# Performance work log

Measured on AMD Instinct MI355X. Metric: run time of the kernel, lower is better.

Reference implementation:

```python
import jax, jax.numpy as jnp
import numpy as np
from jax import lax

IN_CH, FEAT, EMB, P = 384, 256, 32, 64
OUT_CH = (256, 512, 1024, 1024)
EPS_BN = 1e-5


def _conv(x, w, b, stride=1, pad=1, groups=1):
    # x: (B,C,H,W), w: (O, C//groups, kh, kw) torch OIHW layout
    y = lax.conv_general_dilated(x, w, (stride, stride), ((pad, pad), (pad, pad)),
                                 dimension_numbers=('NCHW', 'OIHW', 'NCHW'),
                                 feature_group_count=groups)
    return y + b[None, :, None, None]


def _bn(x, g, b, m, v):
    scale = (g / jnp.sqrt(v + EPS_BN))[None, :, None, None]
    return (x - m[None, :, None, None]) * scale + b[None, :, None, None]


def _convT_block(x, w, b, k):
    # ConvTranspose2d with kernel_size == stride == k, padding 0 (non-overlapping)
    # w: (C_in, C_out, k, k) torch layout
    B, C, H, W = x.shape
    O = w.shape[1]
    y = jnp.einsum('bchw,coij->bohiwj', x, w).reshape(B, O, H * k, W * k)
    return y + b[None, :, None, None]


def _resize_ac(x, oh, ow):
    # bilinear interpolation, align_corners=True; x: (B,C,H,W)
    H, W = x.shape[-2], x.shape[-1]
    def idx(n_in, n_out):
        c = jnp.arange(n_out, dtype=x.dtype) * ((n_in - 1) / max(n_out - 1, 1))
        i0 = jnp.clip(jnp.floor(c).astype(jnp.int32), 0, max(n_in - 2, 0))
        return i0, c - i0.astype(x.dtype)
    if oh != H:
        i0, t = idx(H, oh)
        x = x[:, :, i0, :] * (1.0 - t)[:, None] + x[:, :, jnp.minimum(i0 + 1, H - 1), :] * t[:, None]
    if ow != W:
        j0, t = idx(W, ow)
        x = x[:, :, :, j0] * (1.0 - t) + x[:, :, :, jnp.minimum(j0 + 1, W - 1)] * t
    return x


def _avg3(x):
    # F.avg_pool2d(k=3, s=1, p=1) with count_include_pad=True -> always /9
    s = lax.reduce_window(x, jnp.float32(0.0), lax.add, (1, 1, 3, 3), (1, 1, 1, 1),
                          ((0, 0), (0, 0), (1, 1), (1, 1)))
    return s / 9.0


def _forward(tokens0, tokens1, tokens2, tokens3,
             proj_w0, proj_b0, proj_w1, proj_b1, proj_w2, proj_b2, proj_w3, proj_b3,
             up_w0, up_b0, up_w1, up_b1, down_w3, down_b3,
             fuse_w, fuse_b,
             pe_w1, pe_b1, pe_bn_g, pe_bn_b, pe_bn_m, pe_bn_v, pe_w2, pe_b2,
             prototypes, prototype_biases, bias_scale,
             smooth_w, smooth_b,
             head_w1, head_b1, hbn1_g, hbn1_b, hbn1_m, hbn1_v,
             head_w2, head_b2, hbn2_g, hbn2_b, hbn2_m, hbn2_v,
             head_w3, head_b3, residual_scale,
             patch_h, patch_w):
    B = tokens0.shape[0]
    toks = (tokens0, tokens1, tokens2, tokens3)
    proj = ((proj_w0, proj_b0), (proj_w1, proj_b1), (proj_w2, proj_b2), (proj_w3, proj_b3))
    feats = []
    for t, (w, b) in zip(toks, proj):
        x = t.transpose(0, 2, 1).reshape(B, t.shape[-1], patch_h, patch_w)
        x = jnp.einsum('bchw,oc->bohw', x, w[:, :, 0, 0]) + b[None, :, None, None]  # 1x1 proj
        feats.append(x)
    f0 = _convT_block(feats[0], up_w0, up_b0, 4)
    f1 = _convT_block(feats[1], up_w1, up_b1, 2)
    f2 = feats[2]                                         # identity
    f3 = _conv(feats[3], down_w3, down_b3, stride=2)
    th, tw = f0.shape[-2], f0.shape[-1]
    fused = jnp.concatenate([f0, _resize_ac(f1, th, tw), _resize_ac(f2, th, tw), _resize_ac(f3, th, tw)], axis=1)
    path1 = jax.nn.relu(jnp.einsum('bchw,oc->bohw', fused, fuse_w[:, :, 0, 0]) + fuse_b[None, :, None, None])
    H, W = patch_h * 14, patch_w * 14
    path1 = _resize_ac(path1, H, W)
    pe = _conv(path1, pe_w1, pe_b1)
    pe = jax.nn.relu(_bn(pe, pe_bn_g, pe_bn_b, pe_bn_m, pe_bn_v))
    pe = _conv(pe, pe_w2, pe_b2)                          # (B, EMB, H, W)
    sim = jnp.einsum('behw,pe->bphw', pe, prototypes) / jnp.sqrt(jnp.float32(pe.shape[1]))
    # edge map from embedding gradients, replicate-padded
    gx = jnp.abs(pe[:, :, :, :-1] - pe[:, :, :, 1:])
    gy = jnp.abs(pe[:, :, :-1, :] - pe[:, :, 1:, :])
    gx = jnp.concatenate([gx, gx[:, :, :, -1:]], axis=3)
    gy = jnp.concatenate([gy, gy[:, :, -1:, :]], axis=2)
    edge = (gx.mean(axis=1, keepdims=True) + gy.mean(axis=1, keepdims=True)) * 0.5
    mask = (edge > edge.mean()).astype(pe.dtype)
    for _ in range(2):  # fixed 2-step edge-aware smoothing
        sim = mask * sim + (1.0 - mask) * _avg3(sim)
    # first softmax over prototypes -> entropy regularizer
    act1 = jax.nn.softmax(sim, axis=1)
    activation_entropy = -(act1 * jnp.log(act1 + 1e-8)).sum(axis=1).mean()
    # spatial smoothing conv then second softmax over prototypes
    sim = _conv(sim, smooth_w, smooth_b)
    act = jax.nn.softmax(sim, axis=1)                     # (B, P, H, W)
    bb = 1.0 + jnp.tanh(prototype_biases) * bias_scale    # (P,)
    base_biases = jnp.broadcast_to(bb[None, :], (B, bb.shape[0]))
    base_gain = jnp.einsum('bphw,p->bhw', act, bb)[:, None]  # (B,1,H,W)
    # 64 per-prototype residual heads == grouped convs with groups=P
    n_proto = act.shape[1]
    h = jax.nn.relu(_bn(_conv(act, head_w1, head_b1, groups=n_proto), hbn1_g, hbn1_b, hbn1_m, hbn1_v))
    h = jax.nn.relu(_bn(_conv(h, head_w2, head_b2, groups=n_proto), hbn2_g, hbn2_b, hbn2_m, hbn2_v))
    res = _conv(h, head_w3, head_b3, groups=n_proto)      # (B, P, H, W)
    weighted = (act * res).sum(axis=1, keepdims=True)
    gain = base_gain * (1.0 + jnp.tanh(weighted) * residual_scale)
    instance_bias_map = jnp.clip(gain, 0.5, 2.0)
    return instance_bias_map, act, base_biases, weighted, pe, activation_entropy


def setup_inputs() -> dict:
    key = jax.random.key(0)
    B, N, PH, PW = 2, 256, 16, 16
    ks = iter(jax.random.split(key, 48))
    def rnd(shape, s=1.0):
        return jax.random.normal(next(ks), shape, dtype=jnp.float32) * s
    inp = {}
    for i in range(4):
        inp['tokens%d' % i] = rnd((B, N, IN_CH))
    for i, oc in enumerate(OUT_CH):
        inp['proj_w%d' % i] = rnd((oc, IN_CH, 1, 1), 0.02)
        inp['proj_b%d' % i] = rnd((oc,), 0.01)
    inp['up_w0'] = rnd((OUT_CH[0], OUT_CH[0], 4, 4), 0.02)
    inp['up_b0'] = rnd((OUT_CH[0],), 0.01)
    inp['up_w1'] = rnd((OUT_CH[1], OUT_CH[1], 2, 2), 0.02)
    inp['up_b1'] = rnd((OUT_CH[1],), 0.01)
    inp['down_w3'] = rnd((OUT_CH[3], OUT_CH[3], 3, 3), 0.01)
    inp['down_b3'] = rnd((OUT_CH[3],), 0.01)
    inp['fuse_w'] = rnd((FEAT, sum(OUT_CH), 1, 1), 0.01)
    inp['fuse_b'] = rnd((FEAT,), 0.01)
    inp['pe_w1'] = rnd((FEAT // 2, FEAT, 3, 3), 0.02)
    inp['pe_b1'] = rnd((FEAT // 2,), 0.01)
    inp['pe_bn_g'] = 1.0 + rnd((FEAT // 2,), 0.1)
    inp['pe_bn_b'] = rnd((FEAT // 2,), 0.01)
    inp['pe_bn_m'] = rnd((FEAT // 2,), 0.01)
    inp['pe_bn_v'] = jnp.ones((FEAT // 2,), jnp.float32)
    inp['pe_w2'] = rnd((EMB, FEAT // 2, 3, 3), 0.02)
    inp['pe_b2'] = rnd((EMB,), 0.01)
    inp['prototypes'] = rnd((P, EMB), 0.01)
    inp['prototype_biases'] = rnd((P,), 0.1)
    inp['bias_scale'] = jnp.asarray(0.2, jnp.float32)
    inp['smooth_w'] = rnd((P, P, 3, 3), 0.02)
    inp['smooth_b'] = rnd((P,), 0.01)
    inp['head_w1'] = rnd((P * 8, 1, 3, 3), 0.1)
    inp['head_b1'] = rnd((P * 8,), 0.01)
    inp['hbn1_g'] = 1.0 + rnd((P * 8,), 0.1)
    inp['hbn1_b'] = rnd((P * 8,), 0.01)
    inp['hbn1_m'] = rnd((P * 8,), 0.01)
    inp['hbn1_v'] = jnp.ones((P * 8,), jnp.float32)
    inp['head_w2'] = rnd((P * 8, 8, 3, 3), 0.1)
    inp['head_b2'] = rnd((P * 8,), 0.01)
    inp['hbn2_g'] = 1.0 + rnd((P * 8,), 0.1)
    inp['hbn2_b'] = rnd((P * 8,), 0.01)
    inp['hbn2_m'] = rnd((P * 8,), 0.01)
    inp['hbn2_v'] = jnp.ones((P * 8,), jnp.float32)
    inp['head_w3'] = rnd((P, 8, 3, 3), 0.1)
    inp['head_b3'] = rnd((P,), 0.01)
    inp['residual_scale'] = jnp.asarray(0.1, jnp.float32)
    inp['patch_h'] = PH
    inp['patch_w'] = PW
    return inp


def reference(tokens0, tokens1, tokens2, tokens3,
              proj_w0, proj_b0, proj_w1, proj_b1, proj_w2, proj_b2, proj_w3, proj_b3,
              up_w0, up_b0, up_w1, up_b1, down_w3, down_b3,
              fuse_w, fuse_b,
              pe_w1, pe_b1, pe_bn_g, pe_bn_b, pe_bn_m, pe_bn_v, pe_w2, pe_b2,
              prototypes, prototype_biases, bias_scale,
              smooth_w, smooth_b,
              head_w1, head_b1, hbn1_g, hbn1_b, hbn1_m, hbn1_v,
              head_w2, head_b2, hbn2_g, hbn2_b, hbn2_m, hbn2_v,
              head_w3, head_b3, residual_scale,
              patch_h, patch_w):
    return _forward(tokens0, tokens1, tokens2, tokens3,
                    proj_w0, proj_b0, proj_w1, proj_b1, proj_w2, proj_b2, proj_w3, proj_b3,
                    up_w0, up_b0, up_w1, up_b1, down_w3, down_b3,
                    fuse_w, fuse_b,
                    pe_w1, pe_b1, pe_bn_g, pe_bn_b, pe_bn_m, pe_bn_v, pe_w2, pe_b2,
                    prototypes, prototype_biases, bias_scale,
                    smooth_w, smooth_b,
                    head_w1, head_b1, hbn1_g, hbn1_b, hbn1_m, hbn1_v,
                    head_w2, head_b2, hbn2_g, hbn2_b, hbn2_m, hbn2_v,
                    head_w3, head_b3, residual_scale,
                    patch_h, patch_w)
```

## Files before the change

kernel.cpp:

```cpp
#include <hip/hip_runtime.h>
#include <math.h>

#define BATCH 2
#define NTOK 256
#define INCH 384
#define NP 50176
#define HW 224
#define NPROTO 64
#define EMBD 32

#define OFF_FEATS0   0u
#define OFF_FEATS1   131072u
#define OFF_FEATS2   393216u
#define OFF_FEATS3   917504u
#define OFF_TOKT     1441792u
#define OFF_F0       2228224u
#define OFF_F1       4325376u
#define OFF_F3       5373952u
#define OFF_FUSEDBF  5505024u
#define OFF_WD       5505024u
#define OFF_PART     14942208u
#define OFF_P64C     28573696u
#define OFF_P224C    0u
#define OFF_T1       25690112u
#define OFF_SIMA     0u
#define OFF_SIMB     6422528u
#define OFF_EDGE     12845056u
#define OFF_RES      13000000u
#define OFF_WB       13000000u
#define OFF_SHIFT    13200000u
#define OFF_BGAIN    19422528u
#define OFF_BB       19522880u
#define OFF_ACC      19523008u
#define OFF_WF       19523072u
#define OFF_WFUSE    20000000u
#define OFF_WCV0     20500000u
#define OFF_WCV1     21600000u

#define O_IBM 0u
#define O_ACT 100352u
#define O_BB  6522880u
#define O_WT  6523008u
#define O_PE  6623360u
#define O_ENT 9834624u

typedef __attribute__((ext_vector_type(8))) short bf16x8;
typedef __attribute__((ext_vector_type(4))) float f32x4;
typedef __attribute__((ext_vector_type(2))) float f32x2;

__device__ __forceinline__ short f2bf(float f) {
    unsigned u = __float_as_uint(f);
    unsigned r = (u + 0x7fffu + ((u >> 16) & 1u)) >> 16;
    return (short)r;
}
__device__ __forceinline__ float bf2f(short s) {
    return __uint_as_float(((unsigned)(unsigned short)s) << 16);
}

__global__ void k_transpose(const float* __restrict__ in, float* __restrict__ out) {
    int idx = blockIdx.x * 256 + threadIdx.x;
    int n = idx & 255;
    int c = (idx >> 8) % INCH;
    int b = idx / (INCH * NTOK);
    out[idx] = in[(size_t)b * INCH * NTOK + (size_t)n * INCH + c];
}

__global__ __launch_bounds__(256) void k_proj(const float* __restrict__ A,
                                              const float* __restrict__ W,
                                              const float* __restrict__ bias,
                                              float* __restrict__ out, int O) {
    int p = threadIdx.x;
    int o = blockIdx.x, b = blockIdx.y;
    const float* a = A + (size_t)b * INCH * NTOK + p;
    const float* w = W + (size_t)o * INCH;
    float acc = bias[o];
    for (int c = 0; c < INCH; ++c) acc = fmaf(a[(size_t)c * NTOK], w[c], acc);
    out[((size_t)b * O + o) * NTOK + p] = acc;
}

template <int NT>
__global__ __launch_bounds__(256) void k_wcvprep(const float* __restrict__ W,
                                                 float* __restrict__ WP, int C, int M) {
    __shared__ float t[32][33];
    int c0 = blockIdx.x * 32, m0 = blockIdx.y * 32;
    int tx = threadIdx.x & 31, ty = threadIdx.x >> 5;
#pragma unroll
    for (int r = 0; r < 4; ++r) {
        int cl = ty + r * 8;
        t[cl][tx] = W[(size_t)(c0 + cl) * M + m0 + tx];
    }
    __syncthreads();
    for (int i = threadIdx.x; i < 1024; i += 256) {
        int ml = i % NT;
        int tmp = i / NT;
        int cl = tmp & 31;
        int mh = tmp >> 5;
        WP[(size_t)(m0 / NT + mh) * C * NT + (size_t)(c0 + cl) * NT + ml] = t[cl][mh * NT + ml];
    }
}

template <int NT, int CCH, int K>
__global__ __launch_bounds__(256) void k_convt2(const float* __restrict__ X,
                                                const float* __restrict__ WP,
                                                const float* __restrict__ bias,
                                                float* __restrict__ out,
                                                int C, int O) {
    __shared__ float sX[CCH * 256];
    int tid = threadIdx.x;
    int nt = blockIdx.x, b = blockIdx.y;
    float acc[NT];
#pragma unroll
    for (int j = 0; j < NT; ++j) acc[j] = 0.f;
    const float* Xb = X + (size_t)b * C * 256;
    for (int cc = 0; cc < C; cc += CCH) {
        __syncthreads();
        const f32x4* Xg4 = (const f32x4*)(Xb + (size_t)cc * 256);
        f32x4* s4 = (f32x4*)sX;
        for (int i = tid; i < CCH * 64; i += 256) s4[i] = Xg4[i];
        __syncthreads();
        const float* wr = WP + ((size_t)nt * C + cc) * NT;
        for (int c = 0; c < CCH; ++c) {
            float xv = sX[c * 256 + tid];
            const float* w = wr + c * NT;
#pragma unroll
            for (int j = 0; j < NT; ++j) acc[j] = fmaf(xv, w[j], acc[j]);
        }
    }
    int h = tid >> 4, w = tid & 15;
    int S = 16 * K;
#pragma unroll
    for (int j = 0; j < NT; ++j) {
        int m = nt * NT + j;
        int o = m / (K * K);
        int ij = m - o * (K * K);
        int ii = ij / K, jj = ij - ii * K;
        out[((size_t)b * O + o) * (size_t)(S * S) + (h * K + ii) * S + (w * K + jj)] =
            acc[j] + bias[o];
    }
}

__global__ __launch_bounds__(256) void k_wdprep(const float* __restrict__ W,
                                                float* __restrict__ WP) {
    __shared__ float t[32][33];
    int k0 = blockIdx.x * 32, o0 = blockIdx.y * 32;
    int tx = threadIdx.x & 31, ty = threadIdx.x >> 5;
#pragma unroll
    for (int r = 0; r < 4; ++r) {
        int orow = ty + r * 8;
        t[orow][tx] = W[(size_t)(o0 + orow) * 9216 + k0 + tx];
    }
    __syncthreads();
#pragma unroll
    for (int r = 0; r < 4; ++r) {
        int krow = ty + r * 8;
        int o = o0 + tx;
        WP[(size_t)(o >> 6) * 589824 + (size_t)(k0 + krow) * 64 + (o & 63)] = t[tx][krow];
    }
}

__global__ __launch_bounds__(256) void k_down2(const float* __restrict__ X,
                                               const float* __restrict__ WP,
                                               float* __restrict__ part) {
    __shared__ float sX[64 * 256];
    int tid = threadIdx.x;
    int ot = blockIdx.x, kc = blockIdx.y, b = blockIdx.z;
    int c0 = kc * 64;
    const float* Xg = X + ((size_t)b * 1024 + c0) * 256;
    for (int i = tid; i < 16384; i += 256) {
        int c = i >> 8, px = i & 255;
        int sy = px >> 4, sx = px & 15;
        int par = (sy & 1) * 2 + (sx & 1);
        sX[(c * 4 + par) * 64 + (sy >> 1) * 8 + (sx >> 1)] = Xg[i];
    }
    __syncthreads();
    int lane = tid & 63;
    int w = __builtin_amdgcn_readfirstlane(tid >> 6);
    int oh = lane >> 3, ow = lane & 7;
    int loff[9]; float lmsk[9];
#pragma unroll
    for (int kh = 0; kh < 3; ++kh)
#pragma unroll
        for (int kw = 0; kw < 3; ++kw) {
            int py = (kh == 1) ? 0 : 1;
            int pxp = (kw == 1) ? 0 : 1;
            int u = oh - ((kh == 0) ? 1 : 0);
            int v = ow - ((kw == 0) ? 1 : 0);
            float m = (u >= 0 && v >= 0) ? 1.f : 0.f;
            if (u < 0) u = 0;
            if (v < 0) v = 0;
            loff[kh * 3 + kw] = (py * 2 + pxp) * 64 + u * 8 + v;
            lmsk[kh * 3 + kw] = m;
        }
    float acc[16];
#pragma unroll
    for (int j = 0; j < 16; ++j) acc[j] = 0.f;
    const float* wb = WP + (size_t)ot * 589824 + (size_t)c0 * 576 + w * 16;
    for (int c = 0; c < 64; ++c) {
        const float* xb = sX + c * 256;
        const float* wc = wb + (size_t)c * 576;
#pragma unroll
        for (int tap = 0; tap < 9; ++tap) {
            float xv = xb[loff[tap]] * lmsk[tap];
            const float* wr = wc + tap * 64;
#pragma unroll
            for (int j = 0; j < 16; ++j) acc[j] = fmaf(xv, wr[j], acc[j]);
        }
    }
    float* pp = part + ((size_t)((kc * 2 + b) * 1024 + ot * 64 + w * 16)) * 64 + lane;
#pragma unroll
    for (int j = 0; j < 16; ++j) pp[(size_t)j * 64] = acc[j];
}

__global__ __launch_bounds__(256) void k_downred(const float* __restrict__ part,
                                                 const float* __restrict__ bias,
                                                 float* __restrict__ out) {
    int idx = blockIdx.x * 256 + threadIdx.x;
    int o = (idx >> 6) & 1023;
    int b = idx >> 16;
    int px = idx & 63;
    float s = bias[o];
#pragma unroll
    for (int kcs = 0; kcs < 16; ++kcs)
        s += part[((size_t)(kcs * 2 + b) * 1024 + o) * 64 + px];
    out[idx] = s;
}

__global__ void k_fusedcat_bf(const float* __restrict__ f0, const float* __restrict__ f1,
                              const float* __restrict__ f2, const float* __restrict__ f3,
                              short* __restrict__ out) {
    int idx = blockIdx.x * 256 + threadIdx.x;
    int ch = idx % 2816;
    int t = idx / 2816;
    int pos = t & 4095;
    int b = t >> 12;
    float v;
    if (ch < 256) {
        v = f0[((size_t)(b * 256 + ch)) * 4096 + pos];
    } else {
        const float* src; int sh;
        if (ch < 768)       { src = f1 + ((size_t)(b * 512 + (ch - 256))) * 1024; sh = 32; }
        else if (ch < 1792) { src = f2 + ((size_t)(b * 1024 + (ch - 768))) * 256; sh = 16; }
        else                { src = f3 + ((size_t)(b * 1024 + (ch - 1792))) * 64; sh = 8;  }
        int y = pos >> 6, x = pos & 63;
        float r = (float)(sh - 1) / 63.0f;
        float cy = y * r, cx = x * r;
        int i0 = (int)cy; if (i0 > sh - 2) i0 = sh - 2;
        int j0 = (int)cx; if (j0 > sh - 2) j0 = sh - 2;
        float ty = cy - (float)i0, tx = cx - (float)j0;
        const float* s0 = src + i0 * sh + j0;
        float v00 = s0[0], v01 = s0[1], v10 = s0[sh], v11 = s0[sh + 1];
        float c0 = v00 + ty * (v10 - v00);
        float c1 = v01 + ty * (v11 - v01);
        v = c0 + tx * (c1 - c0);
    }
    out[idx] = f2bf(v);
}

__global__ void k_wfuseprep(const float* __restrict__ w, short* __restrict__ wb) {
    int idx = blockIdx.x * 256 + threadIdx.x;
    int j = idx & 7;
    int lane = (idx >> 3) & 63;
    int ntile = (idx >> 9) & 15;
    int chunk = idx >> 13;
    int oc = ntile * 16 + (lane & 15);
    int c = chunk * 32 + (lane >> 4) * 8 + j;
    wb[idx] = f2bf(w[(size_t)oc * 2816 + c]);
}

__global__ __launch_bounds__(256) void k_fuse_mfma(const short* __restrict__ A,
                                                   const bf16x8* __restrict__ WB,
                                                   const float* __restrict__ bias,
                                                   short* __restrict__ out) {
    int tid = threadIdx.x;
    int lane = tid & 63, w = tid >> 6;
    int row0 = blockIdx.x * 16;
    int l15 = lane & 15, q = lane >> 4;
    int arow = row0 + l15;
    f32x4 acc[4];
#pragma unroll
    for (int nn = 0; nn < 4; ++nn) acc[nn] = (f32x4){0.f, 0.f, 0.f, 0.f};
    const short* arp = A + (size_t)arow * 2816 + q * 8;
    for (int chunk = 0; chunk < 88; ++chunk) {
        bf16x8 a = *(const bf16x8*)(arp + chunk * 32);
        const bf16x8* wbp = WB + ((size_t)(chunk * 16 + w * 4) * 64) + lane;
#pragma unroll
        for (int nn = 0; nn < 4; ++nn) {
            bf16x8 bf = wbp[nn * 64];
            acc[nn] = __builtin_amdgcn_mfma_f32_16x16x32_bf16(a, bf, acc[nn], 0, 0, 0);
        }
    }
#pragma unroll
    for (int nn = 0; nn < 4; ++nn) {
        int oc = (w * 4 + nn) * 16 + l15;
        float bs = bias[oc];
#pragma unroll
        for (int r = 0; r < 4; ++r) {
            int m = q * 4 + r;
            out[(size_t)(row0 + m) * 256 + oc] = f2bf(fmaxf(acc[nn][r] + bs, 0.f));
        }
    }
}

__global__ void k_resize224bf2(const short* __restrict__ in, short* __restrict__ out) {
    int idx = blockIdx.x * 256 + threadIdx.x;
    int c8 = (idx & 31) * 8;
    int p = idx >> 5;
    int b = p / NP;
    int pos = p - b * NP;
    int y = pos / HW, x = pos - y * HW;
    const float r = (float)(63.0 / 223.0);
    float cy = y * r, cx = x * r;
    int i0 = (int)cy; if (i0 > 62) i0 = 62;
    int j0 = (int)cx; if (j0 > 62) j0 = 62;
    float ty = cy - (float)i0, tx = cx - (float)j0;
    const short* base = in + ((size_t)b * 4096) * 256 + c8;
    const bf16x8 v00 = *(const bf16x8*)(base + (size_t)(i0 * 64 + j0) * 256);
    const bf16x8 v01 = *(const bf16x8*)(base + (size_t)(i0 * 64 + j0 + 1) * 256);
    const bf16x8 v10 = *(const bf16x8*)(base + (size_t)((i0 + 1) * 64 + j0) * 256);
    const bf16x8 v11 = *(const bf16x8*)(base + (size_t)((i0 + 1) * 64 + j0 + 1) * 256);
    bf16x8 o;
#pragma unroll
    for (int k = 0; k < 8; ++k) {
        float a00 = bf2f(v00[k]), a01 = bf2f(v01[k]);
        float a10 = bf2f(v10[k]), a11 = bf2f(v11[k]);
        float c0 = a00 + ty * (a10 - a00);
        float c1 = a01 + ty * (a11 - a01);
        o[k] = f2bf(c0 + tx * (c1 - c0));
    }
    *(bf16x8*)(out + ((size_t)b * NP + pos) * 256 + c8) = o;
}

__global__ void k_w1prep(const float* __restrict__ w, const float* __restrict__ bias,
                         const float* __restrict__ g, const float* __restrict__ bb,
                         const float* __restrict__ m, const float* __restrict__ v,
                         short* __restrict__ wb, float* __restrict__ shift) {
    int idx = blockIdx.x * 256 + threadIdx.x;
    int j = idx & 7;
    int lane = (idx >> 3) & 63;
    int nt = (idx >> 9) & 7;
    int tc = idx >> 12;
    int tap = tc % 9, chunk = tc / 9;
    int oc = nt * 16 + (lane & 15);
    int c = chunk * 32 + (lane >> 4) * 8 + j;
    float s = g[oc] * rsqrtf(v[oc] + 1e-5f);
    wb[idx] = f2bf(w[((size_t)oc * 256 + c) * 9 + tap] * s);
    if (idx < 128) {
        float si = g[idx] * rsqrtf(v[idx] + 1e-5f);
        shift[idx] = (bias[idx] - m[idx]) * si + bb[idx];
    }
}

__global__ __launch_bounds__(256) void k_conv1mfma(const short* __restrict__ X,
                                                   const bf16x8* __restrict__ WB,
                                                   const float* __restrict__ shift,
                                                   float* __restrict__ out) {
    int tid = threadIdx.x;
    int lane = tid & 63, w = tid >> 6;
    int t = blockIdx.x;
    int b = blockIdx.y;
    int ty0 = (t / 28) * 16, tx0 = (t % 28) * 8;
    int l15 = lane & 15, q = lane >> 4;
    int loc0 = w * 32 + l15;
    int loc1 = loc0 + 16;
    int py0 = ty0 + (loc0 >> 3), px0 = tx0 + (loc0 & 7);
    int py1 = ty0 + (loc1 >> 3), px1 = tx0 + (loc1 & 7);
    int csub = q * 8;
    f32x4 acc0[8], acc1[8];
#pragma unroll
    for (int nt = 0; nt < 8; ++nt) {
        acc0[nt] = (f32x4){0.f, 0.f, 0.f, 0.f};
        acc1[nt] = (f32x4){0.f, 0.f, 0.f, 0.f};
    }
    const short* Xb = X + (size_t)b * NP * 256;
    const bf16x8 zv = {0, 0, 0, 0, 0, 0, 0, 0};
    for (int chunk = 0; chunk < 8; ++chunk) {
        int c0 = chunk * 32 + csub;
#pragma unroll
        for (int tap = 0; tap < 9; ++tap) {
            int dy = tap / 3 - 1, dx = tap % 3 - 1;
            int sy0 = py0 + dy, sx0 = px0 + dx;
            int sy1 = py1 + dy, sx1 = px1 + dx;
            bf16x8 a0 = zv, a1 = zv;
            if ((unsigned)sy0 < HW && (unsigned)sx0 < HW)
                a0 = *(const bf16x8*)(Xb + ((size_t)sy0 * HW + sx0) * 256 + c0);
            if ((unsigned)sy1 < HW && (unsigned)sx1 < HW)
                a1 = *(const bf16x8*)(Xb + ((size_t)sy1 * HW + sx1) * 256 + c0);
            const bf16x8* wbp = WB + (size_t)((chunk * 9 + tap) * 8) * 64 + lane;
#pragma unroll
            for (int nt = 0; nt < 8; ++nt) {
                bf16x8 bf = wbp[nt * 64];
                acc0[nt] = __builtin_amdgcn_mfma_f32_16x16x32_bf16(a0, bf, acc0[nt], 0, 0, 0);
                acc1[nt] = __builtin_amdgcn_mfma_f32_16x16x32_bf16(a1, bf, acc1[nt], 0, 0, 0);
            }
        }
    }
    int m0 = w * 32, m1 = w * 32 + 16;
#pragma unroll
    for (int nt = 0; nt < 8; ++nt) {
        int oc = nt * 16 + l15;
        float sh = shift[oc];
        float* ob = out + ((size_t)(b * 128 + oc)) * NP;
#pragma unroll
        for (int r = 0; r < 4; ++r) {
            int md = q * 4 + r;
            int lm = m0 + md;
            int py = ty0 + (lm >> 3), px = tx0 + (lm & 7);
            ob[py * HW + px] = fmaxf(acc0[nt][r] + sh, 0.f);
            lm = m1 + md;
            py = ty0 + (lm >> 3); px = tx0 + (lm & 7);
            ob[py * HW + px] = fmaxf(acc1[nt][r] + sh, 0.f);
        }
    }
}

template <int OCT, bool BN, bool RELU>
__global__ __launch_bounds__(256) void k_conv3(const float* __restrict__ in,
                                               const float* __restrict__ W,
                                               const float* __restrict__ bias,
                                               const float* __restrict__ bng,
                                               const float* __restrict__ bnb,
                                               const float* __restrict__ bnm,
                                               const float* __restrict__ bnv,
                                               float* __restrict__ out, int C, int O) {
    int tid = threadIdx.x;
    int tb = blockIdx.x;
    int ty = (tb / 7) * 32, tx = (tb % 7) * 32;
    int o0 = blockIdx.y * OCT;
    int b = blockIdx.z;
    int gx = tx + (tid & 15) * 2;
    int gy = ty + (tid >> 4) * 2;

    int roff[4], coff[4];
    float rmsk[4], cmsk[4];
#pragma unroll
    for (int i = 0; i < 4; ++i) {
        int sy = gy + i - 1;
        rmsk[i] = (sy >= 0 && sy < HW) ? 1.f : 0.f;
        roff[i] = min(max(sy, 0), HW - 1) * HW;
        int sx = gx + i - 1;
        cmsk[i] = (sx >= 0 && sx < HW) ? 1.f : 0.f;
        coff[i] = min(max(sx, 0), HW - 1);
    }
    float acc[OCT][4];
#pragma unroll
    for (int u = 0; u < OCT; ++u)
#pragma unroll
        for (int qq = 0; qq < 4; ++qq) acc[u][qq] = 0.f;

    const float* ic = in + (size_t)b * C * NP;
    const float* wbase = W + (size_t)o0 * C * 9;
    for (int c = 0; c < C; ++c) {
        float r[4][4];
#pragma unroll
        for (int i = 0; i < 4; ++i) {
            float m = rmsk[i];
#pragma unroll
            for (int j = 0; j < 4; ++j)
                r[i][j] = ic[roff[i] + coff[j]] * (m * cmsk[j]);
        }
        const float* wc = wbase + (size_t)c * 9;
#pragma unroll
        for (int u = 0; u < OCT; ++u) {
            const float* w = wc + (size_t)u * C * 9;
            float w0 = w[0], w1 = w[1], w2 = w[2];
            float w3 = w[3], w4 = w[4], w5 = w[5];
            float w6 = w[6], w7 = w[7], w8 = w[8];
            acc[u][0] = fmaf(r[0][0], w0, fmaf(r[0][1], w1, fmaf(r[0][2], w2,
                        fmaf(r[1][0], w3, fmaf(r[1][1], w4, fmaf(r[1][2], w5,
                        fmaf(r[2][0], w6, fmaf(r[2][1], w7, fmaf(r[2][2], w8, acc[u][0])))))))));
            acc[u][1] = fmaf(r[0][1], w0, fmaf(r[0][2], w1, fmaf(r[0][3], w2,
                        fmaf(r[1][1], w3, fmaf(r[1][2], w4, fmaf(r[1][3], w5,
                        fmaf(r[2][1], w6, fmaf(r[2][2], w7, fmaf(r[2][3], w8, acc[u][1])))))))));
            acc[u][2] = fmaf(r[1][0], w0, fmaf(r[1][1], w1, fmaf(r[1][2], w2,
                        fmaf(r[2][0], w3, fmaf(r[2][1], w4, fmaf(r[2][2], w5,
                        fmaf(r[3][0], w6, fmaf(r[3][1], w7, fmaf(r[3][2], w8, acc[u][2])))))))));
            acc[u][3] = fmaf(r[1][1], w0, fmaf(r[1][2], w1, fmaf(r[1][3], w2,
                        fmaf(r[2][1], w3, fmaf(r[2][2], w4, fmaf(r[2][3], w5,
                        fmaf(r[3][1], w6, fmaf(r[3][2], w7, fmaf(r[3][3], w8, acc[u][3])))))))));
        }
        ic += NP;
    }
    size_t obase = (size_t)b * O * NP + (size_t)gy * HW + gx;
#pragma unroll
    for (int u = 0; u < OCT; ++u) {
        int o = o0 + u;
        float bs = bias[o], sc = 1.f, sh = 0.f;
        if (BN) { sc = bng[o] * rsqrtf(bnv[o] + 1e-5f); sh = bnb[o] - bnm[o] * sc; }
        size_t ob = obase + (size_t)o * NP;
#pragma unroll
        for (int qq = 0; qq < 4; ++qq) {
            float v = acc[u][qq] + bs;
            if (BN) v = v * sc + sh;
            if (RELU) v = fmaxf(v, 0.f);
            out[ob + (qq >> 1) * HW + (qq & 1)] = v;
        }
    }
}

__global__ __launch_bounds__(256) void k_sim(const float* __restrict__ pe,
                                             const float* __restrict__ proto,
                                             float* __restrict__ sim) {
    int idx = blockIdx.x * 256 + threadIdx.x;
    int b = idx / NP, pos = idx - b * NP;
    const float* p = pe + (size_t)b * EMBD * NP + pos;
    float v[EMBD];
#pragma unroll
    for (int e = 0; e < EMBD; ++e) v[e] = p[(size_t)e * NP];
    const float scale = 1.0f / sqrtf(32.0f);
    float* so = sim + (size_t)b * NPROTO * NP + pos;
    for (int q = 0; q < NPROTO; ++q) {
        float acc = 0.f;
#pragma unroll
        for (int e = 0; e < EMBD; ++e) acc = fmaf(v[e], proto[q * EMBD + e], acc);
        so[(size_t)q * NP] = acc * scale;
    }
}

__global__ void k_init(float* acc) { if (threadIdx.x < 8) acc[threadIdx.x] = 0.f; }

__device__ __forceinline__ float block_reduce_sum(float v) {
    __shared__ float sh[4];
#pragma unroll
    for (int off = 32; off > 0; off >>= 1) v += __shfl_down(v, off);
    int lane = threadIdx.x & 63, wv = threadIdx.x >> 6;
    if (lane == 0) sh[wv] = v;
    __syncthreads();
    return (threadIdx.x == 0) ? (sh[0] + sh[1] + sh[2] + sh[3]) : 0.f;
}

__global__ __launch_bounds__(256) void k_edge(const float* __restrict__ pe,
                                              float* __restrict__ edge,
                                              float* __restrict__ acc) {
    int idx = blockIdx.x * 256 + threadIdx.x;
    int b = idx / NP, pos = idx - b * NP;
    int h = pos / HW, w = pos - h * HW;
    int wn = (w < HW - 1) ? w : HW - 2;
    int hn = (h < HW - 1) ? h : HW - 2;
    const float* pb = pe + (size_t)b * EMBD * NP;
    float sx = 0.f, sy = 0.f;
#pragma unroll 4
    for (int e = 0; e < EMBD; ++e) {
        const float* p = pb + (size_t)e * NP;
        sx += fabsf(p[h * HW + wn] - p[h * HW + wn + 1]);
        sy += fabsf(p[hn * HW + w] - p[hn * HW + HW + w]);
    }
    float ev = (sx + sy) * (0.5f / 32.0f);
    edge[idx] = ev;
    float tot = block_reduce_sum(ev);
    if (threadIdx.x == 0) atomicAdd(acc, tot);
}

__global__ void k_smooth(const float* __restrict__ sin_, const float* __restrict__ edge,
                         const float* __restrict__ acc, float* __restrict__ sout) {
    int idx = blockIdx.x * 256 + threadIdx.x;
    int pos = idx % NP;
    int bp = idx / NP;
    int b = bp >> 6;
    int h = pos / HW, w = pos - h * HW;
    float mean = acc[0] * (1.0f / 100352.0f);
    float m = (edge[(size_t)b * NP + pos] > mean) ? 1.f : 0.f;
    const float* sc = sin_ + (size_t)bp * NP;
    float s = 0.f;
#pragma unroll
    for (int dy = -1; dy <= 1; ++dy) {
        int yy = h + dy;
        if (yy < 0 || yy >= HW) continue;
#pragma unroll
        for (int dx = -1; dx <= 1; ++dx) {
            int xx = w + dx;
            if (xx < 0 || xx >= HW) continue;
            s += sc[yy * HW + xx];
        }
    }
    float c = sc[pos];
    sout[idx] = m * c + (1.f - m) * (s * (1.0f / 9.0f));
}

__global__ __launch_bounds__(256) void k_entropy(const float* __restrict__ sim,
                                                 float* __restrict__ acc) {
    int idx = blockIdx.x * 256 + threadIdx.x;
    int b = idx / NP, pos = idx - b * NP;
    const float* s = sim + (size_t)b * NPROTO * NP + pos;
    float v[NPROTO];
    float mx = -3.0e38f;
#pragma unroll
    for (int q = 0; q < NPROTO; ++q) { v[q] = s[(size_t)q * NP]; mx = fmaxf(mx, v[q]); }
    float sum = 0.f;
#pragma unroll
    for (int q = 0; q < NPROTO; ++q) { float e = expf(v[q] - mx); v[q] = e; sum += e; }
    float inv = 1.f / sum;
    float ent = 0.f;
#pragma unroll
    for (int q = 0; q < NPROTO; ++q) {
        float a = v[q] * inv;
        ent -= a * logf(a + 1e-8f);
    }
    float tot = block_reduce_sum(ent);
    if (threadIdx.x == 0) atomicAdd(acc + 1, tot);
}

__global__ void k_bb(const float* __restrict__ pb, const float* __restrict__ bs,
                     float* __restrict__ bbuf, float* __restrict__ obb) {
    int t = threadIdx.x;
    if (t < NPROTO) {
        float v = 1.f + tanhf(pb[t]) * bs[0];
        bbuf[t] = v;
        obb[t] = v;
        obb[NPROTO + t] = v;
    }
}

__global__ __launch_bounds__(256) void k_actsm(const float* __restrict__ sim,
                                               const float* __restrict__ bb,
                                               float* __restrict__ act,
                                               float* __restrict__ bgain) {
    int idx = blockIdx.x * 256 + threadIdx.x;
    int b = idx / NP, pos = idx - b * NP;
    const float* s = sim + (size_t)b * NPROTO * NP + pos;
    float v[NPROTO];
    float mx = -3.0e38f;
#pragma unroll
    for (int q = 0; q < NPROTO; ++q) { v[q] = s[(size_t)q * NP]; mx = fmaxf(mx, v[q]); }
    float sum = 0.f;
#pragma unroll
    for (int q = 0; q < NPROTO; ++q) { float e = expf(v[q] - mx); v[q] = e; sum += e; }
    float inv = 1.f / sum;
    float* a = act + (size_t)b * NPROTO * NP + pos;
    float bg = 0.f;
#pragma unroll
    for (int q = 0; q < NPROTO; ++q) {
        float p = v[q] * inv;
        a[(size_t)q * NP] = p;
        bg = fmaf(p, bb[q], bg);
    }
    bgain[idx] = bg;
}

__global__ void k_headprep(const float* __restrict__ w1, const float* __restrict__ b1,
                           const float* __restrict__ g1, const float* __restrict__ be1,
                           const float* __restrict__ m1, const float* __restrict__ v1,
                           const float* __restrict__ w2, const float* __restrict__ b2,
                           const float* __restrict__ g2, const float* __restrict__ be2,
                           const float* __restrict__ m2, const float* __restrict__ v2,
                           float* __restrict__ wf) {
    int oc = blockIdx.x * 256 + threadIdx.x;
    if (oc >= 512) return;
    float s1 = g1[oc] * rsqrtf(v1[oc] + 1e-5f);
#pragma unroll
    for (int k = 0; k < 9; ++k) wf[oc * 9 + k] = w1[oc * 9 + k] * s1;
    wf[41472 + oc] = (b1[oc] - m1[oc]) * s1 + be1[oc];
    float s2 = g2[oc] * rsqrtf(v2[oc] + 1e-5f);
    int g = oc >> 3, j = oc & 7;
#pragma unroll
    for (int icc = 0; icc < 8; ++icc)
#pragma unroll
        for (int k = 0; k < 9; ++k)
            wf[4608 + (size_t)g * 576 + icc * 72 + j * 9 + k] = w2[((size_t)oc * 8 + icc) * 9 + k] * s2;
    wf[41984 + oc] = (b2[oc] - m2[oc]) * s2 + be2[oc];
}

__global__ __launch_bounds__(256) void k_heads(
    const float* __restrict__ act, const float* __restrict__ wf,
    const float* __restrict__ w3, const float* __restrict__ b3,
    float* __restrict__ res) {
    __shared__ float sA[22 * 24];
    __shared__ float sH1[8][20 * 22];
    __shared__ float sH2[8][18 * 18];
    int tid = threadIdx.x;
    int tile = blockIdx.x, g = blockIdx.y, b = blockIdx.z;
    int oy0 = (tile / 14) * 16, ox0 = (tile % 14) * 16;
    const float* ain = act + (size_t)(b * NPROTO + g) * NP;

    for (int i = tid; i < 484; i += 256) {
        int y = i / 22, x = i - y * 22;
        int gy = oy0 - 3 + y, gx = ox0 - 3 + x;
        float v = 0.f;
        if ((unsigned)gy < HW && (unsigned)gx < HW) v = ain[gy * HW + gx];
        sA[y * 24 + x] = v;
    }
    __syncthreads();

    const float* b1f = wf + 41472 + g * 8;
    for (int i = tid; i < 400; i += 256) {
        int y = i / 20, x = i - y * 20;
        int gy = oy0 - 2 + y, gx = ox0 - 2 + x;
        float keep = ((unsigned)gy < HW && (unsigned)gx < HW) ? 1.f : 0.f;
        const float* s0 = sA + y * 24 + x;
        float r0 = s0[0],  r1 = s0[1],  r2 = s0[2];
        float r3 = s0[24], r4 = s0[25], r5 = s0[26];
        float r6 = s0[48], r7 = s0[49], r8 = s0[50];
#pragma unroll
        for (int j = 0; j < 8; ++j) {
            const float* w = wf + (g * 8 + j) * 9;
            float v = fmaf(r0, w[0], fmaf(r1, w[1], fmaf(r2, w[2],
                      fmaf(r3, w[3], fmaf(r4, w[4], fmaf(r5, w[5],
                      fmaf(r6, w[6], fmaf(r7, w[7], fmaf(r8, w[8], b1f[j])))))))));
            sH1[j][y * 22 + x] = fmaxf(v, 0.f) * keep;
        }
    }
    __syncthreads();

    const float* w2f = wf + 4608 + (size_t)g * 576;
    const float* b2f = wf + 41984 + g * 8;
    if (tid < 162) {
        int y2 = tid / 9, xp = (tid - y2 * 9) * 2;
        f32x2 a2[8];
#pragma unroll
        for (int j = 0; j < 8; ++j) { float bv = b2f[j]; a2[j] = (f32x2){bv, bv}; }
#pragma unroll
        for (int icc = 0; icc < 8; ++icc) {
            const float* s0 = &sH1[icc][y2 * 22 + xp];
            f32x2 t[9];
#pragma unroll
            for (int r = 0; r < 3; ++r) {
                float f0 = s0[r * 22], f1 = s0[r * 22 + 1];
                float f2 = s0[r * 22 + 2], f3 = s0[r * 22 + 3];
                t[r * 3 + 0] = (f32x2){f0, f1};
                t[r * 3 + 1] = (f32x2){f1, f2};
                t[r * 3 + 2] = (f32x2){f2, f3};
            }
            const float* wr = w2f + icc * 72;
#pragma unroll
            for (int j = 0; j < 8; ++j) {
                const float* wj = wr + j * 9;
#pragma unroll
                for (int k = 0; k < 9; ++k) {
                    float wv = wj[k];
                    a2[j] = __builtin_elementwise_fma(t[k], (f32x2){wv, wv}, a2[j]);
                }
            }
        }
        int gy = oy0 - 1 + y2;
        int gx0 = ox0 - 1 + xp;
        float k0 = ((unsigned)gy < HW && (unsigned)gx0 < HW) ? 1.f : 0.f;
        float k1 = ((unsigned)gy < HW && (unsigned)(gx0 + 1) < HW) ? 1.f : 0.f;
        f32x2 kp = (f32x2){k0, k1};
        const f32x2 z2 = (f32x2){0.f, 0.f};
#pragma unroll
        for (int j = 0; j < 8; ++j) {
            f32x2 v = __builtin_elementwise_max(a2[j], z2) * kp;
            sH2[j][y2 * 18 + xp] = v.x;
            sH2[j][y2 * 18 + xp + 1] = v.y;
        }
    }
    __syncthreads();

    if (tid < 128) {
        int y3 = tid >> 3, xp = (tid & 7) * 2;
        float bv = b3[g];
        f32x2 a2 = (f32x2){bv, bv};
#pragma unroll
        for (int icc = 0; icc < 8; ++icc) {
            const float* s0 = &sH2[icc][y3 * 18 + xp];
            const float* w = w3 + (size_t)(g * 8 + icc) * 9;
#pragma unroll
            for (int r = 0; r < 3; ++r) {
                float f0 = s0[r * 18], f1 = s0[r * 18 + 1];
                float f2 = s0[r * 18 + 2], f3 = s0[r * 18 + 3];
                float w0 = w[r * 3], w1 = w[r * 3 + 1], w2v = w[r * 3 + 2];
                a2 = __builtin_elementwise_fma((f32x2){f0, f1}, (f32x2){w0, w0}, a2);
                a2 = __builtin_elementwise_fma((f32x2){f1, f2}, (f32x2){w1, w1}, a2);
                a2 = __builtin_elementwise_fma((f32x2){f2, f3}, (f32x2){w2v, w2v}, a2);
            }
        }
        float* rp = res + (size_t)(b * NPROTO + g) * NP + (size_t)(oy0 + y3) * HW + (ox0 + xp);
        rp[0] = a2.x;
        rp[1] = a2.y;
    }
}

__global__ __launch_bounds__(256) void k_final(const float* __restrict__ act,
                                               const float* __restrict__ res,
                                               const float* __restrict__ bgain,
                                               const float* __restrict__ rscale,
                                               float* __restrict__ owt,
                                               float* __restrict__ oibm) {
    int idx = blockIdx.x * 256 + threadIdx.x;
    int b = idx / NP, pos = idx - b * NP;
    const float* a = act + (size_t)b * NPROTO * NP + pos;
    const float* r = res + (size_t)b * NPROTO * NP + pos;
    float wt = 0.f;
#pragma unroll
    for (int q = 0; q < NPROTO; ++q) wt = fmaf(a[(size_t)q * NP], r[(size_t)q * NP], wt);
    owt[idx] = wt;
    float gn = bgain[idx] * (1.f + tanhf(wt) * rscale[0]);
    gn = fminf(fmaxf(gn, 0.5f), 2.0f);
    oibm[idx] = gn;
}

__global__ void k_entfinal(const float* __restrict__ acc, float* __restrict__ o) {
    if (threadIdx.x == 0) o[0] = acc[1] * (1.0f / 100352.0f);
}

extern "C" void kernel_launch(void* const* d_in, const int* in_sizes, int n_in,
                              void* d_out, int out_size, void* d_ws, size_t ws_size,
                              hipStream_t stream) {
    const float* tokens[4] = {(const float*)d_in[0], (const float*)d_in[1],
                              (const float*)d_in[2], (const float*)d_in[3]};
    const float* proj_w[4] = {(const float*)d_in[4], (const float*)d_in[6],
                              (const float*)d_in[8], (const float*)d_in[10]};
    const float* proj_b[4] = {(const float*)d_in[5], (const float*)d_in[7],
                              (const float*)d_in[9], (const float*)d_in[11]};
    const float* up_w0 = (const float*)d_in[12]; const float* up_b0 = (const float*)d_in[13];
    const float* up_w1 = (const float*)d_in[14]; const float* up_b1 = (const float*)d_in[15];
    const float* down_w3 = (const float*)d_in[16]; const float* down_b3 = (const float*)d_in[17];
    const float* fuse_w = (const float*)d_in[18]; const float* fuse_b = (const float*)d_in[19];
    const float* pe_w1 = (const float*)d_in[20]; const float* pe_b1 = (const float*)d_in[21];
    const float* pe_bn_g = (const float*)d_in[22]; const float* pe_bn_b = (const float*)d_in[23];
    const float* pe_bn_m = (const float*)d_in[24]; const float* pe_bn_v = (const float*)d_in[25];
    const float* pe_w2 = (const float*)d_in[26]; const float* pe_b2 = (const float*)d_in[27];
    const float* prototypes = (const float*)d_in[28];
    const float* proto_biases = (const float*)d_in[29];
    const float* bias_scale = (const float*)d_in[30];
    const float* smooth_w = (const float*)d_in[31]; const float* smooth_b = (const float*)d_in[32];
    const float* hw1 = (const float*)d_in[33]; const float* hb1 = (const float*)d_in[34];
    const float* hg1 = (const float*)d_in[35]; const float* hbe1 = (const float*)d_in[36];
    const float* hm1 = (const float*)d_in[37]; const float* hv1 = (const float*)d_in[38];
    const float* hw2 = (const float*)d_in[39]; const float* hb2 = (const float*)d_in[40];
    const float* hg2 = (const float*)d_in[41]; const float* hbe2 = (const float*)d_in[42];
    const float* hm2 = (const float*)d_in[43]; const float* hv2 = (const float*)d_in[44];
    const float* hw3 = (const float*)d_in[45]; const float* hb3 = (const float*)d_in[46];
    const float* rscale = (const float*)d_in[47];
    (void)in_sizes; (void)n_in; (void)out_size; (void)ws_size;

    float* ws = (float*)d_ws;
    float* FEATS[4] = {ws + OFF_FEATS0, ws + OFF_FEATS1, ws + OFF_FEATS2, ws + OFF_FEATS3};
    float* TOKT = ws + OFF_TOKT;
    float* F0 = ws + OFF_F0; float* F1 = ws + OFF_F1; float* F3 = ws + OFF_F3;
    short* FUSEDBF = (short*)(ws + OFF_FUSEDBF);
    short* P64C = (short*)(ws + OFF_P64C);
    short* P224C = (short*)(ws + OFF_P224C);
    short* WB = (short*)(ws + OFF_WB);
    short* WFUSE = (short*)(ws + OFF_WFUSE);
    float* SHIFT = ws + OFF_SHIFT;
    float* T1 = ws + OFF_T1;
    float* SIMA = ws + OFF_SIMA; float* SIMB = ws + OFF_SIMB;
    float* EDGE = ws + OFF_EDGE; float* RES = ws + OFF_RES;
    float* BGAIN = ws + OFF_BGAIN; float* BBUF = ws + OFF_BB; float* ACC = ws + OFF_ACC;
    float* WF = ws + OFF_WF;
    float* WDP = ws + OFF_WD;
    float* PART = ws + OFF_PART;
    float* WCV0 = ws + OFF_WCV0;
    float* WCV1 = ws + OFF_WCV1;

    float* out = (float*)d_out;
    float* o_ibm = out + O_IBM; float* o_act = out + O_ACT; float* o_bb = out + O_BB;
    float* o_wt = out + O_WT; float* o_pe = out + O_PE; float* o_ent = out + O_ENT;

    const int OCH[4] = {256, 512, 1024, 1024};
    for (int s = 0; s < 4; ++s)
        k_transpose<<<768, 256, 0, stream>>>(tokens[s], TOKT + s * 196608);
    for (int s = 0; s < 4; ++s)
        k_proj<<<dim3(OCH[s], BATCH), 256, 0, stream>>>(TOKT + s * 196608, proj_w[s], proj_b[s],
                                                        FEATS[s], OCH[s]);
    k_wcvprep<16><<<dim3(8, 128), 256, 0, stream>>>(up_w0, WCV0, 256, 4096);
    k_wcvprep<8><<<dim3(16, 64), 256, 0, stream>>>(up_w1, WCV1, 512, 2048);
    k_convt2<16, 64, 4><<<dim3(256, BATCH), 256, 0, stream>>>(FEATS[0], WCV0, up_b0, F0, 256, 256);
    k_convt2<8, 64, 2><<<dim3(256, BATCH), 256, 0, stream>>>(FEATS[1], WCV1, up_b1, F1, 512, 512);
    k_wdprep<<<dim3(288, 32), 256, 0, stream>>>(down_w3, WDP);
    k_down2<<<dim3(16, 16, BATCH), 256, 0, stream>>>(FEATS[3], WDP, PART);
    k_downred<<<512, 256, 0, stream>>>(PART, down_b3, F3);
    k_wfuseprep<<<2816, 256, 0, stream>>>(fuse_w, WFUSE);
    k_fusedcat_bf<<<90112, 256, 0, stream>>>(F0, F1, FEATS[2], F3, FUSEDBF);
    k_fuse_mfma<<<512, 256, 0, stream>>>(FUSEDBF, (const bf16x8*)WFUSE, fuse_b, P64C);
    k_w1prep<<<1152, 256, 0, stream>>>(pe_w1, pe_b1, pe_bn_g, pe_bn_b, pe_bn_m, pe_bn_v,
                                       WB, SHIFT);
    k_resize224bf2<<<12544, 256, 0, stream>>>(P64C, P224C);
    k_conv1mfma<<<dim3(392, BATCH), 256, 0, stream>>>(P224C, (const bf16x8*)WB, SHIFT, T1);
    k_conv3<4, false, false><<<dim3(49, 8, BATCH), 256, 0, stream>>>(
        T1, pe_w2, pe_b2, nullptr, nullptr, nullptr, nullptr, o_pe, 128, 32);
    k_sim<<<392, 256, 0, stream>>>(o_pe, prototypes, SIMA);
    k_init<<<1, 64, 0, stream>>>(ACC);
    k_edge<<<392, 256, 0, stream>>>(o_pe, EDGE, ACC);
    k_smooth<<<25088, 256, 0, stream>>>(SIMA, EDGE, ACC, SIMB);
    k_smooth<<<25088, 256, 0, stream>>>(SIMB, EDGE, ACC, SIMA);
    k_entropy<<<392, 256, 0, stream>>>(SIMA, ACC);
    k_conv3<8, false, false><<<dim3(49, 8, BATCH), 256, 0, stream>>>(
        SIMA, smooth_w, smooth_b, nullptr, nullptr, nullptr, nullptr, SIMB, 64, 64);
    k_bb<<<1, 64, 0, stream>>>(proto_biases, bias_scale, BBUF, o_bb);
    k_actsm<<<392, 256, 0, stream>>>(SIMB, BBUF, o_act, BGAIN);
    k_headprep<<<2, 256, 0, stream>>>(hw1, hb1, hg1, hbe1, hm1, hv1,
                                      hw2, hb2, hg2, hbe2, hm2, hv2, WF);
    k_heads<<<dim3(196, 64, BATCH), 256, 0, stream>>>(o_act, WF, hw3, hb3, RES);
    k_final<<<392, 256, 0, stream>>>(o_act, RES, BGAIN, rscale, o_wt, o_ibm);
    k_entfinal<<<1, 1, 0, stream>>>(ACC, o_ent);
}
```

Before: 1.735 ms.

## Rewrite 3x3 convs with LDS-staged input tiles and all-output-channel register blocking

Replaces the direct global-memory 3x3 conv with a kernel that stages 16x16+halo input tiles for chunks of channels in shared memory. Each thread computes one pixel for all output channels, with weights pre-transposed to [c][tap][o] so the inner loop reads them uniformly. The goal is to stop re-reading each input channel once per output-channel group and to cut redundant global loads. The cost is fewer blocks (392), per-thread register arrays of 32 or 64 accumulators, and two extra weight-prep launches.

```diff
diff --git a/kernel.cpp b/kernel.cpp
--- a/kernel.cpp
+++ b/kernel.cpp
@@ -36,6 +36,8 @@
 #define OFF_WFUSE    20000000u
 #define OFF_WCV0     20500000u
 #define OFF_WCV1     21600000u
+#define OFF_WC2      22700000u
+#define OFF_WSM      22750000u
 
 #define O_IBM 0u
 #define O_ACT 100352u
@@ -413,88 +415,64 @@
     }
 }
 
-template <int OCT, bool BN, bool RELU>
-__global__ __launch_bounds__(256) void k_conv3(const float* __restrict__ in,
-                                               const float* __restrict__ W,
-                                               const float* __restrict__ bias,
-                                               const float* __restrict__ bng,
-                                               const float* __restrict__ bnb,
-                                               const float* __restrict__ bnm,
-                                               const float* __restrict__ bnv,
-                                               float* __restrict__ out, int C, int O) {
+__global__ void k_wc3prep(const float* __restrict__ W, float* __restrict__ WP,
+                          int C, int O) {
+    int idx = blockIdx.x * 256 + threadIdx.x;
+    if (idx >= C * 9 * O) return;
+    int o = idx % O;
+    int t = idx / O;
+    int tap = t % 9, c = t / 9;
+    WP[idx] = W[((size_t)o * C + c) * 9 + tap];
+}
+
+template <int O, int C, int CCH>
+__global__ __launch_bounds__(256) void k_conv3v2(const float* __restrict__ in,
+                                                 const float* __restrict__ WP,
+                                                 const float* __restrict__ bias,
+                                                 float* __restrict__ out) {
+    __shared__ float sX[CCH * 324];
     int tid = threadIdx.x;
-    int tb = blockIdx.x;
-    int ty = (tb / 7) * 32, tx = (tb % 7) * 32;
-    int o0 = blockIdx.y * OCT;
-    int b = blockIdx.z;
-    int gx = tx + (tid & 15) * 2;
-    int gy = ty + (tid >> 4) * 2;
-
-    int roff[4], coff[4];
-    float rmsk[4], cmsk[4];
-#pragma unroll
-    for (int i = 0; i < 4; ++i) {
-        int sy = gy + i - 1;
-        rmsk[i] = (sy >= 0 && sy < HW) ? 1.f : 0.f;
-        roff[i] = min(max(sy, 0), HW - 1) * HW;
-        int sx = gx + i - 1;
-        cmsk[i] = (sx >= 0 && sx < HW) ? 1.f : 0.f;
-        coff[i] = min(max(sx, 0), HW - 1);
-    }
-    float acc[OCT][4];
-#pragma unroll
-    for (int u = 0; u < OCT; ++u)
-#pragma unroll
-        for (int qq = 0; qq < 4; ++qq) acc[u][qq] = 0.f;
-
+    int tb = blockIdx.x, b = blockIdx.y;
+    int ty0 = (tb / 14) * 16, tx0 = (tb % 14) * 16;
+    int px = tid & 15, py = tid >> 4;
+    float acc[O];
+#pragma unroll
+    for (int o = 0; o < O; ++o) acc[o] = 0.f;
     const float* ic = in + (size_t)b * C * NP;
-    const float* wbase = W + (size_t)o0 * C * 9;
-    for (int c = 0; c < C; ++c) {
-        float r[4][4];
-#pragma unroll
-        for (int i = 0; i < 4; ++i) {
-            float m = rmsk[i];
-#pragma unroll
-            for (int j = 0; j < 4; ++j)
-                r[i][j] = ic[roff[i] + coff[j]] * (m * cmsk[j]);
-        }
-        const float* wc = wbase + (size_t)c * 9;
-#pragma unroll
-        for (int u = 0; u < OCT; ++u) {
-            const float* w = wc + (size_t)u * C * 9;
-            float w0 = w[0], w1 = w[1], w2 = w[2];
-            float w3 = w[3], w4 = w[4], w5 = w[5];
-            float w6 = w[6], w7 = w[7], w8 = w[8];
-            acc[u][0] = fmaf(r[0][0], w0, fmaf(r[0][1], w1, fmaf(r[0][2], w2,
-                        fmaf(r[1][0], w3, fmaf(r[1][1], w4, fmaf(r[1][2], w5,
-                        fmaf(r[2][0], w6, fmaf(r[2][1], w7, fmaf(r[2][2], w8, acc[u][0])))))))));
-            acc[u][1] = fmaf(r[0][1], w0, fmaf(r[0][2], w1, fmaf(r[0][3], w2,
-                        fmaf(r[1][1], w3, fmaf(r[1][2], w4, fmaf(r[1][3], w5,
-                        fmaf(r[2][1], w6, fmaf(r[2][2], w7, fmaf(r[2][3], w8, acc[u][1])))))))));
-            acc[u][2] = fmaf(r[1][0], w0, fmaf(r[1][1], w1, fmaf(r[1][2], w2,
-                        fmaf(r[2][0], w3, fmaf(r[2][1], w4, fmaf(r[2][2], w5,
-                        fmaf(r[3][0], w6, fmaf(r[3][1], w7, fmaf(r[3][2], w8, acc[u][2])))))))));
-            acc[u][3] = fmaf(r[1][1], w0, fmaf(r[1][2], w1, fmaf(r[1][3], w2,
-                        fmaf(r[2][1], w3, fmaf(r[2][2], w4, fmaf(r[2][3], w5,
-                        fmaf(r[3][1], w6, fmaf(r[3][2], w7, fmaf(r[3][3], w8, acc[u][3])))))))));
-        }
-        ic += NP;
-    }
-    size_t obase = (size_t)b * O * NP + (size_t)gy * HW + gx;
-#pragma unroll
-    for (int u = 0; u < OCT; ++u) {
-        int o = o0 + u;
-        float bs = bias[o], sc = 1.f, sh = 0.f;
-        if (BN) { sc = bng[o] * rsqrtf(bnv[o] + 1e-5f); sh = bnb[o] - bnm[o] * sc; }
-        size_t ob = obase + (size_t)o * NP;
-#pragma unroll
-        for (int qq = 0; qq < 4; ++qq) {
-            float v = acc[u][qq] + bs;
-            if (BN) v = v * sc + sh;
-            if (RELU) v = fmaxf(v, 0.f);
-            out[ob + (qq >> 1) * HW + (qq & 1)] = v;
-        }
-    }
+    for (int cc = 0; cc < C; cc += CCH) {
+        __syncthreads();
+        for (int i = tid; i < CCH * 324; i += 256) {
+            int c = i / 324;
+            int r = i - c * 324;
+            int y = r / 18, x = r - y * 18;
+            int sy = ty0 + y - 1, sx = tx0 + x - 1;
+            float v = 0.f;
+            if ((unsigned)sy < HW && (unsigned)sx < HW)
+                v = ic[(size_t)(cc + c) * NP + sy * HW + sx];
+            sX[i] = v;
+        }
+        __syncthreads();
+        const float* wr = WP + (size_t)cc * 9 * O;
+        const float* xb = sX + py * 18 + px;
+#pragma unroll 1
+        for (int c = 0; c < CCH; ++c) {
+            const float* xc = xb + c * 324;
+            const float* wc = wr + (size_t)c * 9 * O;
+#pragma unroll
+            for (int kh = 0; kh < 3; ++kh)
+#pragma unroll
+                for (int kw = 0; kw < 3; ++kw) {
+                    float xv = xc[kh * 18 + kw];
+                    const float* wt = wc + (kh * 3 + kw) * O;
+#pragma unroll
+                    for (int o = 0; o < O; ++o) acc[o] = fmaf(xv, wt[o], acc[o]);
+                }
+        }
+    }
+    int gy = ty0 + py, gx = tx0 + px;
+    float* ob = out + (size_t)b * O * NP + (size_t)gy * HW + gx;
+#pragma unroll
+    for (int o = 0; o < O; ++o) ob[(size_t)o * NP] = acc[o] + bias[o];
 }
 
 __global__ __launch_bounds__(256) void k_sim(const float* __restrict__ pe,
@@ -842,6 +820,8 @@
     float* PART = ws + OFF_PART;
     float* WCV0 = ws + OFF_WCV0;
     float* WCV1 = ws + OFF_WCV1;
+    float* WC2 = ws + OFF_WC2;
+    float* WSM = ws + OFF_WSM;
 
     float* out = (float*)d_out;
     float* o_ibm = out + O_IBM; float* o_act = out + O_ACT; float* o_bb = out + O_BB;
@@ -860,6 +840,8 @@
     k_wdprep<<<dim3(288, 32), 256, 0, stream>>>(down_w3, WDP);
     k_down2<<<dim3(16, 16, BATCH), 256, 0, stream>>>(FEATS[3], WDP, PART);
     k_downred<<<512, 256, 0, stream>>>(PART, down_b3, F3);
+    k_wc3prep<<<144, 256, 0, stream>>>(pe_w2, WC2, 128, 32);
+    k_wc3prep<<<144, 256, 0, stream>>>(smooth_w, WSM, 64, 64);
     k_wfuseprep<<<2816, 256, 0, stream>>>(fuse_w, WFUSE);
     k_fusedcat_bf<<<90112, 256, 0, stream>>>(F0, F1, FEATS[2], F3, FUSEDBF);
     k_fuse_mfma<<<512, 256, 0, stream>>>(FUSEDBF, (const bf16x8*)WFUSE, fuse_b, P64C);
@@ -867,16 +849,14 @@
                                        WB, SHIFT);
     k_resize224bf2<<<12544, 256, 0, stream>>>(P64C, P224C);
     k_conv1mfma<<<dim3(392, BATCH), 256, 0, stream>>>(P224C, (const bf16x8*)WB, SHIFT, T1);
-    k_conv3<4, false, false><<<dim3(49, 8, BATCH), 256, 0, stream>>>(
-        T1, pe_w2, pe_b2, nullptr, nullptr, nullptr, nullptr, o_pe, 128, 32);
+    k_conv3v2<32, 128, 16><<<dim3(196, BATCH), 256, 0, stream>>>(T1, WC2, pe_b2, o_pe);
     k_sim<<<392, 256, 0, stream>>>(o_pe, prototypes, SIMA);
     k_init<<<1, 64, 0, stream>>>(ACC);
     k_edge<<<392, 256, 0, stream>>>(o_pe, EDGE, ACC);
     k_smooth<<<25088, 256, 0, stream>>>(SIMA, EDGE, ACC, SIMB);
     k_smooth<<<25088, 256, 0, stream>>>(SIMB, EDGE, ACC, SIMA);
     k_entropy<<<392, 256, 0, stream>>>(SIMA, ACC);
-    k_conv3<8, false, false><<<dim3(49, 8, BATCH), 256, 0, stream>>>(
-        SIMA, smooth_w, smooth_b, nullptr, nullptr, nullptr, nullptr, SIMB, 64, 64);
+    k_conv3v2<64, 64, 16><<<dim3(196, BATCH), 256, 0, stream>>>(SIMA, WSM, smooth_b, SIMB);
     k_bb<<<1, 64, 0, stream>>>(proto_biases, bias_scale, BBUF, o_bb);
     k_actsm<<<392, 256, 0, stream>>>(SIMB, BBUF, o_act, BGAIN);
     k_headprep<<<2, 256, 0, stream>>>(hw1, hb1, hg1, hbe1, hm1, hv1,
```

Result: slower. 1.793 ms (+3.4%).
